# Kernel optimization log

Hardware: AMD Instinct MI355X
Metric: run time of the kernel (lower is better)

## Reference

```python
import jax, jax.numpy as jnp
import numpy as np

C, N, H = 24, 1536, 40          # n_clusters, max_cluster_size, max_hull_vertices
SEP_W, T_PEN, R_PEN = 1.0, 0.1, 1.0
EPS = 1e-8


def setup_inputs() -> dict:
    rng = np.random.default_rng(0)
    medoids = rng.uniform(0.0, 100.0, (C, 2)).astype(np.float32)
    pts = np.zeros((C, N, 2), np.float32)
    pmask = np.zeros((C, N), bool)
    hulls = np.zeros((C, H, 2), np.float32)
    hmask = np.zeros((C, H), bool)
    for i in range(C):  # loop over fixed small n_clusters (setup only)
        n = int(rng.integers(N // 2, N + 1))
        pts[i, :n] = medoids[i] + rng.normal(0.0, 5.0, (n, 2))
        pmask[i, :n] = True
        h = int(rng.integers(16, H + 1))
        ang = np.sort(rng.uniform(0.0, 2.0 * np.pi, h))
        r = rng.uniform(6.0, 12.0)
        v = (medoids[i] + r * np.stack([np.cos(ang), np.sin(ang)], 1)).astype(np.float32)
        hulls[i, :h] = v
        hulls[i, h:] = v[-1]  # repeat last vertex -> padding edges have zero length
        hmask[i, :h] = True
    k1, k2 = jax.random.split(jax.random.key(0))
    return {
        'padded_clusters': jnp.asarray(pts),
        'padded_hulls': jnp.asarray(hulls),
        'medoids': jnp.asarray(medoids),
        'rotation_angles': 0.1 * jax.random.normal(k1, (C,), jnp.float32),
        'translations': jax.random.normal(k2, (C, 2), jnp.float32),
        'cluster_masks': jnp.asarray(pmask),
        'hull_masks': jnp.asarray(hmask),
    }


def _transform(x, medoids, angles, trans):
    # rotation about medoid, then translate: matches apply_transformations_vectorized
    c, s = jnp.cos(angles), jnp.sin(angles)
    # torch bmm(points, R) with R[k] = [[cos, sin], [-sin, cos]]
    R = jnp.stack([jnp.stack([c, s], -1), jnp.stack([-s, c], -1)], -2)  # (C,2,2)
    centered = x - medoids[:, None, :]
    return jnp.einsum('cnd,cde->cne', centered, R) + (medoids + trans)[:, None, :]


def reference(padded_clusters, padded_hulls, medoids, rotation_angles, translations,
              cluster_masks, hull_masks):
    pts = _transform(padded_clusters, medoids, rotation_angles, translations)  # (C,N,2)
    hul = _transform(padded_hulls, medoids, rotation_angles, translations)     # (C,H,2)

    p1 = hul
    p2 = jnp.roll(hul, -1, axis=1)
    edges = p2 - p1                                   # (C,H,2)
    elen_raw = jnp.linalg.norm(edges, axis=-1)        # (C,H)
    elen = elen_raw + EPS
    evalid = elen_raw > 1e-6                          # skip zero-length padding edges

    ex, ey = edges[..., 0], edges[..., 1]
    c0 = ex * p1[..., 1] - ey * p1[..., 0]            # (C,H)
    px, py = pts[..., 0], pts[..., 1]
    cross = (ex[None, :, None, :] * py[:, None, :, None]
             - ey[None, :, None, :] * px[:, None, :, None]
             - c0[None, :, None, :])                  # (C,C,N,H)
    signed = cross / elen[None, :, None, :]

    v = evalid[None, :, None, :]
    all_pos = jnp.all(jnp.where(v, signed >= -EPS, True), axis=-1)
    all_neg = jnp.all(jnp.where(v, signed <= EPS, True), axis=-1)
    inside = all_pos | all_neg                        # (C,C,N)
    min_abs = jnp.min(jnp.where(v, jnp.abs(signed), jnp.inf), axis=-1)
    viol = jnp.where(inside, jax.nn.sigmoid(min_abs), 0.0)

    hull_ok = jnp.sum(hull_masks, -1) >= 3            # hull_mask.sum() < 3 -> zeros
    offdiag = ~jnp.eye(C, dtype=bool)                 # own hull excluded
    m = cluster_masks[:, None, :] & offdiag[:, :, None] & hull_ok[None, :, None]
    sep = jnp.sum(jnp.where(m, viol, 0.0))

    return (SEP_W * sep
            + T_PEN * jnp.sum(translations ** 2)
            + R_PEN * jnp.sum(rotation_angles ** 2))
```

## Files before the change

kernel.cpp:

```cpp
#include <hip/hip_runtime.h>
#include <math.h>

#define NC    24
#define NPTS  1536
#define NH    40
#define FEPS  1e-8f
#define GROUPS 4
#define JPG    6

__device__ __forceinline__ int mask_fmt(const void* m) {
    int w = ((const int*)m)[0];
    if (w == 1) return 1;
    if (w == 0x3f800000) return 2;
    return 0;
}
__device__ __forceinline__ bool mask_at(const void* m, int idx, int fmt) {
    if (fmt == 1) return ((const int*)m)[idx] != 0;
    if (fmt == 2) return ((const float*)m)[idx] != 0.0f;
    return ((const unsigned char*)m)[idx] != 0;
}

__global__ __launch_bounds__(1024)
void prep_kernel(const float* __restrict__ hulls, const float* __restrict__ med,
                 const float* __restrict__ ang, const float* __restrict__ trans,
                 const void* __restrict__ hmask,
                 float4* __restrict__ edges, int* __restrict__ hok,
                 float* __restrict__ out)
{
    const int tid = threadIdx.x;
    if (tid < NC * NH) {
        const int j = tid / NH, h = tid % NH;
        float sj, cj;
        __sincosf(ang[j], &sj, &cj);
        const float mx = med[2*j], my = med[2*j+1];
        const float tx = trans[2*j], ty = trans[2*j+1];
        const int hn = (h + 1 == NH) ? 0 : h + 1;
        const float x1 = hulls[(j*NH + h )*2], y1 = hulls[(j*NH + h )*2 + 1];
        const float x2 = hulls[(j*NH + hn)*2], y2 = hulls[(j*NH + hn)*2 + 1];
        const float cx1 = x1 - mx, cy1 = y1 - my;
        const float p1x = cx1*cj - cy1*sj + mx + tx;
        const float p1y = cx1*sj + cy1*cj + my + ty;
        const float cx2 = x2 - mx, cy2 = y2 - my;
        const float p2x = cx2*cj - cy2*sj + mx + tx;
        const float p2y = cx2*sj + cy2*cj + my + ty;
        const float ex = p2x - p1x, ey = p2y - p1y;
        const float el = sqrtf(ex*ex + ey*ey);
        const float inv = (el > 1e-6f) ? 1.0f / (el + FEPS) : 0.0f;
        const float c0 = ex*p1y - ey*p1x;
        edges[tid] = make_float4(ex, ey, c0, inv);
    } else if (tid < NC * NH + NC) {
        const int j = tid - NC * NH;
        const int hfmt = mask_fmt(hmask);
        int cnt = 0;
        for (int h = 0; h < NH; ++h) cnt += mask_at(hmask, j*NH + h, hfmt) ? 1 : 0;
        hok[j] = (cnt >= 3) ? 1 : 0;
    } else if (tid == 1023) {
        float pen = 0.f;
        for (int c = 0; c < NC; ++c) {
            const float tx = trans[2*c], ty = trans[2*c+1], a = ang[c];
            pen += 0.1f * (tx*tx + ty*ty) + 1.0f * (a*a);
        }
        atomicAdd(out, pen);
    }
}

__global__ __launch_bounds__(256)
void eval_kernel(const float* __restrict__ pts, const float* __restrict__ med,
                 const float* __restrict__ ang, const float* __restrict__ trans,
                 const void* __restrict__ cmask,
                 const float4* __restrict__ edges, const int* __restrict__ hok,
                 float* __restrict__ out)
{
    const int tid = threadIdx.x;
    const int i = blockIdx.y;
    const int z = blockIdx.z;

    __shared__ float4 s_e[JPG * NH];
    __shared__ int    s_ok[JPG];
    __shared__ float  s_part[4];

    if (tid < JPG * NH) s_e[tid] = edges[z * JPG * NH + tid];
    if (tid < JPG)      s_ok[tid] = hok[z * JPG + tid];
    __syncthreads();

    const int n = blockIdx.x * 256 + tid;
    const int cfmt = mask_fmt(cmask);
    const bool pm = mask_at(cmask, i*NPTS + n, cfmt);
    float si, ci;
    __sincosf(ang[i], &si, &ci);
    const float mx = med[2*i], my = med[2*i+1];
    const float tx = trans[2*i], ty = trans[2*i+1];
    const float x = pts[(i*NPTS + n)*2 + 0];
    const float y = pts[(i*NPTS + n)*2 + 1];
    const float cx = x - mx, cy = y - my;
    const float px = cx*ci - cy*si + mx + tx;
    const float py = cx*si + cy*ci + my + ty;

    float acc = 0.f;
    for (int g = 0; g < JPG; ++g) {
        const int j = z * JPG + g;
        if (j == i || !s_ok[g]) continue;
        bool allpos = true, allneg = true;
        float minabs = INFINITY;
#pragma unroll
        for (int h = 0; h < NH; ++h) {
            const float4 e = s_e[g*NH + h];
            const float cross = fmaf(e.x, py, -fmaf(e.y, px, e.z));
            const float sgn = cross * e.w;
            allpos = allpos && (sgn >= -FEPS);
            allneg = allneg && (sgn <=  FEPS);
            minabs = fminf(minabs, (e.w > 0.f) ? fabsf(sgn) : INFINITY);
        }
        if (allpos || allneg)
            acc += 1.0f / (1.0f + __expf(-minabs));
    }
    if (!pm) acc = 0.f;

#pragma unroll
    for (int off = 32; off > 0; off >>= 1)
        acc += __shfl_down(acc, off, 64);
    const int lane = tid & 63, wid = tid >> 6;
    if (lane == 0) s_part[wid] = acc;
    __syncthreads();
    if (tid == 0) atomicAdd(out, s_part[0] + s_part[1] + s_part[2] + s_part[3]);
}

extern "C" void kernel_launch(void* const* d_in, const int* in_sizes, int n_in,
                              void* d_out, int out_size, void* d_ws, size_t ws_size,
                              hipStream_t stream) {
    const float* pts   = (const float*)d_in[0];
    const float* hulls = (const float*)d_in[1];
    const float* med   = (const float*)d_in[2];
    const float* ang   = (const float*)d_in[3];
    const float* trans = (const float*)d_in[4];
    const void*  cmask = d_in[5];
    const void*  hmask = d_in[6];
    float* out = (float*)d_out;

    float4* edges = (float4*)d_ws;
    int*    hok   = (int*)((char*)d_ws + NC*NH*sizeof(float4));

    hipMemsetAsync(out, 0, sizeof(float), stream);
    prep_kernel<<<1, 1024, 0, stream>>>(hulls, med, ang, trans, hmask, edges, hok, out);
    dim3 grid(NPTS / 256, NC, GROUPS);
    eval_kernel<<<grid, dim3(256, 1, 1), 0, stream>>>(pts, med, ang, trans, cmask,
                                                      edges, hok, out);
}
```

Baseline: 90.41 us.

## Fuse hull edge prep into eval kernel and widen hull grouping grid

Result: faster. 80.56 us (-10.9%).

```diff
diff --git a/kernel.cpp b/kernel.cpp
--- a/kernel.cpp
+++ b/kernel.cpp
@@ -5,8 +5,9 @@
 #define NPTS  1536
 #define NH    40
 #define FEPS  1e-8f
-#define GROUPS 4
-#define JPG    6
+#define GROUPS 12
+#define JPG    2
+#define TPB   256
 
 __device__ __forceinline__ int mask_fmt(const void* m) {
     int w = ((const int*)m)[0];
@@ -20,101 +21,96 @@
     return ((const unsigned char*)m)[idx] != 0;
 }
 
-__global__ __launch_bounds__(1024)
-void prep_kernel(const float* __restrict__ hulls, const float* __restrict__ med,
-                 const float* __restrict__ ang, const float* __restrict__ trans,
-                 const void* __restrict__ hmask,
-                 float4* __restrict__ edges, int* __restrict__ hok,
-                 float* __restrict__ out)
+__global__ __launch_bounds__(TPB)
+void fused_kernel(const float* __restrict__ pts, const float* __restrict__ hulls,
+                  const float* __restrict__ med, const float* __restrict__ ang,
+                  const float* __restrict__ trans,
+                  const void* __restrict__ cmask, const void* __restrict__ hmask,
+                  float* __restrict__ out)
 {
     const int tid = threadIdx.x;
-    if (tid < NC * NH) {
-        const int j = tid / NH, h = tid % NH;
+    const int i  = blockIdx.y;
+    const int z  = blockIdx.z;
+    const int j0 = z * JPG;
+
+    __shared__ float4 s_e[JPG * NH];
+    __shared__ float  s_big[JPG * NH];
+    __shared__ int    s_ok[JPG];
+    __shared__ float  s_part[4];
+
+    if (tid < JPG * NH) {
+        const int g = tid / NH, h = tid - g * NH;
+        const int j = j0 + g;
         float sj, cj;
         __sincosf(ang[j], &sj, &cj);
         const float mx = med[2*j], my = med[2*j+1];
         const float tx = trans[2*j], ty = trans[2*j+1];
         const int hn = (h + 1 == NH) ? 0 : h + 1;
-        const float x1 = hulls[(j*NH + h )*2], y1 = hulls[(j*NH + h )*2 + 1];
-        const float x2 = hulls[(j*NH + hn)*2], y2 = hulls[(j*NH + hn)*2 + 1];
-        const float cx1 = x1 - mx, cy1 = y1 - my;
+        const float2 v1 = ((const float2*)hulls)[j*NH + h ];
+        const float2 v2 = ((const float2*)hulls)[j*NH + hn];
+        const float cx1 = v1.x - mx, cy1 = v1.y - my;
         const float p1x = cx1*cj - cy1*sj + mx + tx;
         const float p1y = cx1*sj + cy1*cj + my + ty;
-        const float cx2 = x2 - mx, cy2 = y2 - my;
+        const float cx2 = v2.x - mx, cy2 = v2.y - my;
         const float p2x = cx2*cj - cy2*sj + mx + tx;
         const float p2y = cx2*sj + cy2*cj + my + ty;
         const float ex = p2x - p1x, ey = p2y - p1y;
         const float el = sqrtf(ex*ex + ey*ey);
-        const float inv = (el > 1e-6f) ? 1.0f / (el + FEPS) : 0.0f;
+        const bool valid = el > 1e-6f;
+        const float inv = valid ? 1.0f / (el + FEPS) : 0.0f;
         const float c0 = ex*p1y - ey*p1x;
-        edges[tid] = make_float4(ex, ey, c0, inv);
-    } else if (tid < NC * NH + NC) {
-        const int j = tid - NC * NH;
+        s_e[tid]   = make_float4(ex, ey, c0, inv);
+        s_big[tid] = valid ? 0.0f : INFINITY;
+    } else if (tid < JPG * NH + JPG) {
+        const int g = tid - JPG * NH;
         const int hfmt = mask_fmt(hmask);
         int cnt = 0;
-        for (int h = 0; h < NH; ++h) cnt += mask_at(hmask, j*NH + h, hfmt) ? 1 : 0;
-        hok[j] = (cnt >= 3) ? 1 : 0;
-    } else if (tid == 1023) {
-        float pen = 0.f;
-        for (int c = 0; c < NC; ++c) {
-            const float tx = trans[2*c], ty = trans[2*c+1], a = ang[c];
-            pen += 0.1f * (tx*tx + ty*ty) + 1.0f * (a*a);
-        }
-        atomicAdd(out, pen);
+        for (int h = 0; h < NH; ++h) cnt += mask_at(hmask, (j0+g)*NH + h, hfmt) ? 1 : 0;
+        s_ok[g] = (cnt >= 3) ? 1 : 0;
     }
-}
-
-__global__ __launch_bounds__(256)
-void eval_kernel(const float* __restrict__ pts, const float* __restrict__ med,
-                 const float* __restrict__ ang, const float* __restrict__ trans,
-                 const void* __restrict__ cmask,
-                 const float4* __restrict__ edges, const int* __restrict__ hok,
-                 float* __restrict__ out)
-{
-    const int tid = threadIdx.x;
-    const int i = blockIdx.y;
-    const int z = blockIdx.z;
-
-    __shared__ float4 s_e[JPG * NH];
-    __shared__ int    s_ok[JPG];
-    __shared__ float  s_part[4];
-
-    if (tid < JPG * NH) s_e[tid] = edges[z * JPG * NH + tid];
-    if (tid < JPG)      s_ok[tid] = hok[z * JPG + tid];
     __syncthreads();
 
-    const int n = blockIdx.x * 256 + tid;
+    const int n = blockIdx.x * TPB + tid;
     const int cfmt = mask_fmt(cmask);
     const bool pm = mask_at(cmask, i*NPTS + n, cfmt);
     float si, ci;
     __sincosf(ang[i], &si, &ci);
     const float mx = med[2*i], my = med[2*i+1];
     const float tx = trans[2*i], ty = trans[2*i+1];
-    const float x = pts[(i*NPTS + n)*2 + 0];
-    const float y = pts[(i*NPTS + n)*2 + 1];
-    const float cx = x - mx, cy = y - my;
+    const float2 p = ((const float2*)pts)[i*NPTS + n];
+    const float cx = p.x - mx, cy = p.y - my;
     const float px = cx*ci - cy*si + mx + tx;
     const float py = cx*si + cy*ci + my + ty;
 
     float acc = 0.f;
     for (int g = 0; g < JPG; ++g) {
-        const int j = z * JPG + g;
+        const int j = j0 + g;
         if (j == i || !s_ok[g]) continue;
-        bool allpos = true, allneg = true;
-        float minabs = INFINITY;
+        float mn = INFINITY, mxs = -INFINITY, ma = INFINITY;
 #pragma unroll
         for (int h = 0; h < NH; ++h) {
-            const float4 e = s_e[g*NH + h];
-            const float cross = fmaf(e.x, py, -fmaf(e.y, px, e.z));
-            const float sgn = cross * e.w;
-            allpos = allpos && (sgn >= -FEPS);
-            allneg = allneg && (sgn <=  FEPS);
-            minabs = fminf(minabs, (e.w > 0.f) ? fabsf(sgn) : INFINITY);
+            const float4 e  = s_e[g*NH + h];
+            const float big = s_big[g*NH + h];
+            const float t  = fmaf(e.y, px, e.z);
+            const float cr = fmaf(e.x, py, -t);
+            const float sg = cr * e.w;
+            mn  = fminf(mn,  sg);
+            mxs = fmaxf(mxs, sg);
+            ma  = fminf(ma, fabsf(sg) + big);
         }
-        if (allpos || allneg)
-            acc += 1.0f / (1.0f + __expf(-minabs));
+        if (mn >= -FEPS || mxs <= FEPS)
+            acc += 1.0f / (1.0f + __expf(-ma));
     }
     if (!pm) acc = 0.f;
+
+    if (blockIdx.x == 0 && i == 0 && z == 0 && tid == TPB - 1) {
+        float pen = 0.f;
+        for (int c = 0; c < NC; ++c) {
+            const float tcx = trans[2*c], tcy = trans[2*c+1], a = ang[c];
+            pen += 0.1f * (tcx*tcx + tcy*tcy) + 1.0f * (a*a);
+        }
+        acc += pen;
+    }
 
 #pragma unroll
     for (int off = 32; off > 0; off >>= 1)
@@ -122,7 +118,10 @@
     const int lane = tid & 63, wid = tid >> 6;
     if (lane == 0) s_part[wid] = acc;
     __syncthreads();
-    if (tid == 0) atomicAdd(out, s_part[0] + s_part[1] + s_part[2] + s_part[3]);
+    if (tid == 0) {
+        const float v = s_part[0] + s_part[1] + s_part[2] + s_part[3];
+        if (v != 0.f) atomicAdd(out, v);
+    }
 }
 
 extern "C" void kernel_launch(void* const* d_in, const int* in_sizes, int n_in,
@@ -137,12 +136,10 @@
     const void*  hmask = d_in[6];
     float* out = (float*)d_out;
 
-    float4* edges = (float4*)d_ws;
-    int*    hok   = (int*)((char*)d_ws + NC*NH*sizeof(float4));
+    (void)d_ws; (void)ws_size;
 
     hipMemsetAsync(out, 0, sizeof(float), stream);
-    prep_kernel<<<1, 1024, 0, stream>>>(hulls, med, ang, trans, hmask, edges, hok, out);
-    dim3 grid(NPTS / 256, NC, GROUPS);
-    eval_kernel<<<grid, dim3(256, 1, 1), 0, stream>>>(pts, med, ang, trans, cmask,
-                                                      edges, hok, out);
+    dim3 grid(NPTS / TPB, NC, GROUPS);
+    fused_kernel<<<grid, dim3(TPB, 1, 1), 0, stream>>>(pts, hulls, med, ang, trans,
+                                                       cmask, hmask, out);
 }
```
